# Kernel tuning notes

Hardware: AMD Instinct MI355X
Metric: run time of the kernel (lower is better)

Reference implementation:

```python
import jax, jax.numpy as jnp
import numpy as np

B, T, S, A, H = 64, 128, 100, 16, 120
TAU = 5.0


def setup_inputs() -> dict:
    key = jax.random.key(0)
    ks = jax.random.split(key, 12)
    kH = 1.0 / np.sqrt(H)
    u = lambda k, shape, b: jax.random.uniform(k, shape, jnp.float32, -b, b)
    return {
        "x": jax.random.normal(ks[0], (B, T, S, A), jnp.float32),
        # PyTorch LSTM params (gate order i, f, g, o), uniform(-1/sqrt(H), 1/sqrt(H))
        "W_ih": u(ks[1], (4 * H, A), kH),
        "W_hh": u(ks[2], (4 * H, H), kH),
        "b_ih": u(ks[3], (4 * H,), kH),
        "b_hh": u(ks[4], (4 * H,), kH),
        # score head: Linear(H, 1)
        "w_lin": u(ks[5], (1, H), kH),
        "b_lin": u(ks[6], (1,), kH),
        # MLP: Linear(S*S, 256), Linear(256, S)
        "W2": u(ks[7], (256, S * S), 1.0 / np.sqrt(S * S)),
        "b2": u(ks[8], (256,), 1.0 / np.sqrt(S * S)),
        "W3": u(ks[9], (S, 256), 1.0 / np.sqrt(256)),
        "b3": u(ks[10], (S,), 1.0 / np.sqrt(256)),
    }


def reference(x, W_ih, W_hh, b_ih, b_hh, w_lin, b_lin, W2, b2, W3, b3):
    Bsz, Tlen, Ns, _ = x.shape
    Hd = W_hh.shape[1]
    # Batch all stocks together: original loops the LSTM per stock with zero init,
    # which is mathematically identical to one LSTM over batch B*S.
    xr = jnp.transpose(x, (1, 0, 2, 3)).reshape(Tlen, Bsz * Ns, -1)  # (T, B*S, A)
    bias = b_ih + b_hh

    def step(carry, xt):
        h, c = carry
        g = xt @ W_ih.T + h @ W_hh.T + bias          # (B*S, 4H)
        i, f, gg, o = jnp.split(g, 4, axis=-1)
        i = jax.nn.sigmoid(i)
        f = jax.nn.sigmoid(f)
        gg = jnp.tanh(gg)
        o = jax.nn.sigmoid(o)
        c = f * c + i * gg
        h = o * jnp.tanh(c)
        return (h, c), None

    h0 = jnp.zeros((Bsz * Ns, Hd), x.dtype)
    (h_last, _), _ = jax.lax.scan(step, (h0, h0), xr)
    lstm_out_last = h_last.reshape(Bsz, Ns, Hd)       # (B, S, H)

    # per-element score linear (batched instead of python double-loop)
    s = lstm_out_last @ w_lin.T + b_lin               # (B, S, 1)

    # NeuralSort relaxed permutation matrix, tau = 5
    A_s = jnp.abs(s - jnp.transpose(s, (0, 2, 1)))    # (B, S, S)
    rowsum = A_s.sum(axis=-1, keepdims=True)          # (B, S, 1) == A_s @ 1 1^T rows
    scaling = (Ns + 1 - 2 * jnp.arange(1, Ns + 1)).astype(x.dtype)  # (S,)
    C = s * scaling[None, None, :]                    # (B, S, S)
    P_max = jnp.transpose(C - rowsum, (0, 2, 1))
    p_hat = jax.nn.softmax(P_max / TAU, axis=-1)      # (B, S, S)

    foo = p_hat.reshape(Bsz, Ns * Ns)
    z = jax.nn.relu(foo @ W2.T + b2)
    z = z @ W3.T + b3
    return jax.nn.softmax(z, axis=-1)                 # (B, S)
```

## Files before the change

kernel.cpp:

```cpp
#include <hip/hip_runtime.h>
#include <hip/hip_bf16.h>
#include <cstddef>

#define NSTOCK 100
#define LOG2E 1.4426950408889634f

typedef _Float16 f16x8 __attribute__((ext_vector_type(8)));
typedef _Float16 f16x4 __attribute__((ext_vector_type(4)));
typedef float f32x16 __attribute__((ext_vector_type(16)));

static __device__ __forceinline__ float rcpf(float x){ return __builtin_amdgcn_rcpf(x); }
static __device__ __forceinline__ float exp2f_(float x){ return __builtin_amdgcn_exp2f(x); }

__global__ void prep_kernel(const float* __restrict__ W_ih,
                            const float* __restrict__ W_hh,
                            const float* __restrict__ b_ih,
                            const float* __restrict__ b_hh,
                            float* __restrict__ Wp) {
    int idx = blockIdx.x * 256 + threadIdx.x;
    if (idx < 480 * 144) {
        int k = idx % 144;
        int p = idx / 144;
        int n = p >> 5, row = p & 31, jjf = row >> 2, type = row & 3;
        int j = n * 8 + (jjf & 1) * 4 + (jjf >> 1);
        int g = type * 120 + j;
        float scale = (type == 2) ? 2.f * LOG2E : -LOG2E;
        float v = 0.f;
        if (k < 136)       v = ((k < 16) ? W_ih[g * 16 + k] : W_hh[g * 120 + (k - 16)]) * scale;
        else if (k == 136) v = (b_ih[g] + b_hh[g]) * scale;
        Wp[idx] = v;
    }
}

__global__ __launch_bounds__(1024) void lstm_kernel(
        const float* __restrict__ x,
        const float* __restrict__ Wp,
        const float* __restrict__ w_lin,
        const float* __restrict__ b_lin,
        float* __restrict__ s_out) {
    __shared__ __align__(16) _Float16 AHi[2][9][64][8];
    __shared__ __align__(16) _Float16 ALoX[2][64][8];
    __shared__ float sred[30][32];

    const int tid   = threadIdx.x;
    const int lane  = tid & 63;
    const int w     = tid >> 6;
    const int l31   = lane & 31;
    const int lhalf = lane >> 5;
    const int n0    = blockIdx.x * 32;

    f16x8 bh[9], bl0;
    if (w < 15) {
        const int p = w * 32 + l31;
#pragma unroll
        for (int kt = 0; kt < 9; ++kt) {
            const float* wp = Wp + p * 144 + kt * 16 + lhalf * 8;
            f16x8 hi, lo;
#pragma unroll
            for (int e = 0; e < 8; ++e) {
                float v = wp[e];
                _Float16 h_ = (_Float16)v;
                hi[e] = h_;
                lo[e] = (_Float16)(v - (float)h_);
            }
            bh[kt] = hi;
            if (kt == 0) bl0 = lo;
        }
    }

    {
        f16x8 z;
#pragma unroll
        for (int e = 0; e < 8; ++e) z[e] = (_Float16)0.f;
        int bf = tid >> 9, kt = 1 + ((tid >> 6) & 7), ln = tid & 63;
        *(f16x8*)&AHi[bf][kt][ln][0] = z;
    }
    __syncthreads();

    const int bx = lane >> 1;
    const int hx = lane & 1;
    const int nx  = n0 + bx;
    const int bbx = nx / NSTOCK, ssx = nx % NSTOCK;
    const float* xbase = x + (size_t)bbx * 204800 + ssx * 16 + hx * 8;
    if (w == 15) {
        float4 a0 = *(const float4*)xbase;
        float4 a1 = *(const float4*)(xbase + 4);
        float vv[8] = {a0.x, a0.y, a0.z, a0.w, a1.x, a1.y, a1.z, a1.w};
        f16x8 hi, lo;
#pragma unroll
        for (int e = 0; e < 8; ++e) {
            _Float16 h_ = (_Float16)vv[e];
            hi[e] = h_; lo[e] = (_Float16)(vv[e] - (float)h_);
        }
        *(f16x8*)&AHi[0][0][bx + 32 * hx][0] = hi;
        *(f16x8*)&ALoX[0][bx + 32 * hx][0] = lo;
    }
    if (tid < 64) {
        int buf = tid >> 5, b = tid & 31;
        AHi[buf][8][32 + b][0] = (_Float16)1.f;
    }
    __syncthreads();

    const int ktw = 1 + (w >> 1);
    const int lnw = l31 + 32 * (w & 1);
    const int e0  = 4 * lhalf;

    float creg[4] = {0.f, 0.f, 0.f, 0.f};
    float hlast[4] = {0.f, 0.f, 0.f, 0.f};

    for (int t = 0; t < 128; ++t) {
        const int rb = t & 1;
        const int wb = rb ^ 1;
        if (w == 15) {
            int tt = (t < 127) ? t + 1 : 127;
            const float* xp = xbase + (size_t)tt * 1600;
            float4 a0 = *(const float4*)xp;
            float4 a1 = *(const float4*)(xp + 4);
            float vv[8] = {a0.x, a0.y, a0.z, a0.w, a1.x, a1.y, a1.z, a1.w};
            f16x8 hi, lo;
#pragma unroll
            for (int e = 0; e < 8; ++e) {
                _Float16 h_ = (_Float16)vv[e];
                hi[e] = h_; lo[e] = (_Float16)(vv[e] - (float)h_);
            }
            *(f16x8*)&AHi[wb][0][bx + 32 * hx][0] = hi;
            *(f16x8*)&ALoX[wb][bx + 32 * hx][0] = lo;
        } else {
            f32x16 acc;
#pragma unroll
            for (int r = 0; r < 16; ++r) acc[r] = 0.f;
            {
                f16x8 ah = *(const f16x8*)&AHi[rb][0][lane][0];
                f16x8 al = *(const f16x8*)&ALoX[rb][lane][0];
                acc = __builtin_amdgcn_mfma_f32_32x32x16_f16(bh[0], ah, acc, 0, 0, 0);
                acc = __builtin_amdgcn_mfma_f32_32x32x16_f16(bh[0], al, acc, 0, 0, 0);
                acc = __builtin_amdgcn_mfma_f32_32x32x16_f16(bl0, ah, acc, 0, 0, 0);
            }
#pragma unroll
            for (int kt = 1; kt < 9; ++kt) {
                f16x8 ah = *(const f16x8*)&AHi[rb][kt][lane][0];
                acc = __builtin_amdgcn_mfma_f32_32x32x16_f16(bh[kt], ah, acc, 0, 0, 0);
            }
            f16x4 hi4;
#pragma unroll
            for (int p = 0; p < 4; ++p) {
                float iv = rcpf(1.f + exp2f_(acc[4 * p + 0]));
                float fv = rcpf(1.f + exp2f_(acc[4 * p + 1]));
                float gv = 1.f - 2.f * rcpf(1.f + exp2f_(acc[4 * p + 2]));
                float ov = rcpf(1.f + exp2f_(acc[4 * p + 3]));
                float c = fv * creg[p] + iv * gv;
                creg[p] = c;
                float h = ov * (1.f - 2.f * rcpf(1.f + exp2f_(c * 2.8853900817779268f)));
                hlast[p] = h;
                hi4[p] = (_Float16)h;
            }
            *(f16x4*)&AHi[wb][ktw][lnw][e0] = hi4;
        }
        __syncthreads();
    }

    if (w < 15) {
        const int jb = w * 8 + 4 * lhalf;
        float sp = 0.f;
#pragma unroll
        for (int p = 0; p < 4; ++p) sp += w_lin[jb + p] * hlast[p];
        sred[w * 2 + lhalf][l31] = sp;
    }
    __syncthreads();
    if (tid < 32) {
        float s = b_lin[0];
#pragma unroll
        for (int r = 0; r < 30; ++r) s += sred[r][tid];
        s_out[n0 + tid] = s;
    }
}

__global__ __launch_bounds__(128) void phat_kernel(const float* __restrict__ s,
                                                   float* __restrict__ fooT) {
    __shared__ float a[NSTOCK], c[NSTOCK];
    const int b = blockIdx.x >> 1, half = blockIdx.x & 1, tid = threadIdx.x;
    const float* sb = s + b * NSTOCK;
    if (tid < NSTOCK) {
        float sj = sb[tid];
        float rs = 0.f;
        for (int i2 = 0; i2 < NSTOCK; ++i2) rs += fabsf(sj - sb[i2]);
        a[tid] = sj * 0.2f;
        c[tid] = rs * 0.2f;
    }
    __syncthreads();
    if (tid < 50) {
        const int i = half * 50 + tid;
        const float sci = (float)(99 - 2 * i);
        float m = -1e30f;
        for (int j = 0; j < NSTOCK; ++j) m = fmaxf(m, sci * a[j] - c[j]);
        float sum = 0.f;
        for (int j = 0; j < NSTOCK; ++j) sum += __expf(sci * a[j] - c[j] - m);
        const float inv = 1.f / sum;
        for (int j = 0; j < NSTOCK; ++j)
            fooT[(size_t)(i * NSTOCK + j) * 64 + b] = __expf(sci * a[j] - c[j] - m) * inv;
    }
}

__global__ __launch_bounds__(512) void mlp1_kernel(const float* __restrict__ fooT,
                                                   const float* __restrict__ W2,
                                                   float* __restrict__ z2Tp) {
    __shared__ float part[8][4][64];
    const int tid = threadIdx.x;
    const int wv = tid >> 6, lane = tid & 63;
    const int ug = blockIdx.x >> 1, half = blockIdx.x & 1;
    const int u0 = ug * 4;
    const int m0 = half * 5000 + wv * 625;
    float a0 = 0.f, a1 = 0.f, a2 = 0.f, a3 = 0.f;
    for (int mi = 0; mi < 625; ++mi) {
        int m = m0 + mi;
        float v = fooT[(size_t)m * 64 + lane];
        a0 += v * W2[(size_t)(u0 + 0) * 10000 + m];
        a1 += v * W2[(size_t)(u0 + 1) * 10000 + m];
        a2 += v * W2[(size_t)(u0 + 2) * 10000 + m];
        a3 += v * W2[(size_t)(u0 + 3) * 10000 + m];
    }
    part[wv][0][lane] = a0; part[wv][1][lane] = a1;
    part[wv][2][lane] = a2; part[wv][3][lane] = a3;
    __syncthreads();
    if (tid < 256) {
        int q = tid >> 6, b = tid & 63;
        float s = 0.f;
#pragma unroll
        for (int w2 = 0; w2 < 8; ++w2) s += part[w2][q][b];
        z2Tp[((size_t)half * 256 + (u0 + q)) * 64 + b] = s;
    }
}

__global__ __launch_bounds__(128) void mlp2_kernel(const float* __restrict__ z2Tp,
                                                   const float* __restrict__ b2,
                                                   const float* __restrict__ W3,
                                                   const float* __restrict__ b3,
                                                   float* __restrict__ out) {
    __shared__ float zs[256];
    __shared__ float logits[NSTOCK];
    const int b = blockIdx.x, tid = threadIdx.x;
    for (int u = tid; u < 256; u += 128) {
        float v = b2[u] + z2Tp[(size_t)u * 64 + b] + z2Tp[(size_t)(256 + u) * 64 + b];
        zs[u] = fmaxf(v, 0.f);
    }
    __syncthreads();
    if (tid < NSTOCK) {
        float acc = b3[tid];
        const float* wr = W3 + tid * 256;
        for (int u = 0; u < 256; ++u) acc += zs[u] * wr[u];
        logits[tid] = acc;
    }
    __syncthreads();
    if (tid < NSTOCK) {
        float m = -1e30f;
        for (int j = 0; j < NSTOCK; ++j) m = fmaxf(m, logits[j]);
        float sum = 0.f;
        for (int j = 0; j < NSTOCK; ++j) sum += __expf(logits[j] - m);
        out[b * NSTOCK + tid] = __expf(logits[tid] - m) / sum;
    }
}

extern "C" void kernel_launch(void* const* d_in, const int* in_sizes, int n_in,
                              void* d_out, int out_size, void* d_ws, size_t ws_size,
                              hipStream_t stream) {
    const float* x     = (const float*)d_in[0];
    const float* W_ih  = (const float*)d_in[1];
    const float* W_hh  = (const float*)d_in[2];
    const float* b_ih  = (const float*)d_in[3];
    const float* b_hh  = (const float*)d_in[4];
    const float* w_lin = (const float*)d_in[5];
    const float* b_lin = (const float*)d_in[6];
    const float* W2    = (const float*)d_in[7];
    const float* b2    = (const float*)d_in[8];
    const float* W3    = (const float*)d_in[9];
    const float* b3    = (const float*)d_in[10];

    float* ws    = (float*)d_ws;
    float* Wp    = ws;
    float* sbuf  = ws + 69600;
    float* fooT  = ws + 76000;
    float* z2Tp  = ws + 716000;
    float* out   = (float*)d_out;

    prep_kernel<<<271, 256, 0, stream>>>(W_ih, W_hh, b_ih, b_hh, Wp);
    lstm_kernel<<<200, 1024, 0, stream>>>(x, Wp, w_lin, b_lin, sbuf);
    phat_kernel<<<128, 128, 0, stream>>>(sbuf, fooT);
    mlp1_kernel<<<128, 512, 0, stream>>>(fooT, W2, z2Tp);
    mlp2_kernel<<<64, 128, 0, stream>>>(z2Tp, b2, W3, b3, out);
}
```

Measured before the change: 254.6 us.

## Interleave two sequence groups per LSTM block and restructure NeuralSort and MLP kernels

The LSTM kernel now processes 64 sequences per block as two independent 32-row groups. Their MFMA chains and gate math interleave, which gives ILP to hide MFMA latency within each serial timestep, and the grid halves to 100 blocks. The p_hat stage is split into a rowsum kernel and a per-row softmax kernel with coalesced 64-wide batch access, and it writes fooT in fp16 to halve traffic into mlp1. mlp1 computes 8 output units per block instead of 4, halving its grid and W2/fooT re-reads. The risks are fewer blocks on a large GPU (100 vs 200 CUs busy), higher register pressure, and fp16 rounding of the p_hat values.

```diff
diff --git a/kernel.cpp b/kernel.cpp
--- a/kernel.cpp
+++ b/kernel.cpp
@@ -38,16 +38,16 @@
         const float* __restrict__ w_lin,
         const float* __restrict__ b_lin,
         float* __restrict__ s_out) {
-    __shared__ __align__(16) _Float16 AHi[2][9][64][8];
-    __shared__ __align__(16) _Float16 ALoX[2][64][8];
-    __shared__ float sred[30][32];
+    __shared__ __align__(16) _Float16 AHi[2][2][9][64][8];
+    __shared__ __align__(16) _Float16 ALoX[2][2][64][8];
+    __shared__ float sred[30][64];
 
     const int tid   = threadIdx.x;
     const int lane  = tid & 63;
     const int w     = tid >> 6;
     const int l31   = lane & 31;
     const int lhalf = lane >> 5;
-    const int n0    = blockIdx.x * 32;
+    const int n0    = blockIdx.x * 64;
 
     f16x8 bh[9], bl0;
     if (w < 15) {
@@ -72,32 +72,38 @@
         f16x8 z;
 #pragma unroll
         for (int e = 0; e < 8; ++e) z[e] = (_Float16)0.f;
-        int bf = tid >> 9, kt = 1 + ((tid >> 6) & 7), ln = tid & 63;
-        *(f16x8*)&AHi[bf][kt][ln][0] = z;
+        for (int ii = tid; ii < 2048; ii += 1024) {
+            int g = ii >> 10, bf = (ii >> 9) & 1, kt = 1 + ((ii >> 6) & 7), ln = ii & 63;
+            *(f16x8*)&AHi[g][bf][kt][ln][0] = z;
+        }
     }
     __syncthreads();
 
     const int bx = lane >> 1;
     const int hx = lane & 1;
-    const int nx  = n0 + bx;
-    const int bbx = nx / NSTOCK, ssx = nx % NSTOCK;
-    const float* xbase = x + (size_t)bbx * 204800 + ssx * 16 + hx * 8;
+    const int rA = n0 + bx, rB = n0 + 32 + bx;
+    const float* xbaseA = x + (size_t)(rA / NSTOCK) * 204800 + (rA % NSTOCK) * 16 + hx * 8;
+    const float* xbaseB = x + (size_t)(rB / NSTOCK) * 204800 + (rB % NSTOCK) * 16 + hx * 8;
     if (w == 15) {
-        float4 a0 = *(const float4*)xbase;
-        float4 a1 = *(const float4*)(xbase + 4);
-        float vv[8] = {a0.x, a0.y, a0.z, a0.w, a1.x, a1.y, a1.z, a1.w};
-        f16x8 hi, lo;
-#pragma unroll
-        for (int e = 0; e < 8; ++e) {
-            _Float16 h_ = (_Float16)vv[e];
-            hi[e] = h_; lo[e] = (_Float16)(vv[e] - (float)h_);
-        }
-        *(f16x8*)&AHi[0][0][bx + 32 * hx][0] = hi;
-        *(f16x8*)&ALoX[0][bx + 32 * hx][0] = lo;
-    }
-    if (tid < 64) {
-        int buf = tid >> 5, b = tid & 31;
-        AHi[buf][8][32 + b][0] = (_Float16)1.f;
+#pragma unroll
+        for (int g = 0; g < 2; ++g) {
+            const float* xb = g ? xbaseB : xbaseA;
+            float4 a0 = *(const float4*)xb;
+            float4 a1 = *(const float4*)(xb + 4);
+            float vv[8] = {a0.x, a0.y, a0.z, a0.w, a1.x, a1.y, a1.z, a1.w};
+            f16x8 hi, lo;
+#pragma unroll
+            for (int e = 0; e < 8; ++e) {
+                _Float16 h_ = (_Float16)vv[e];
+                hi[e] = h_; lo[e] = (_Float16)(vv[e] - (float)h_);
+            }
+            *(f16x8*)&AHi[g][0][0][bx + 32 * hx][0] = hi;
+            *(f16x8*)&ALoX[g][0][bx + 32 * hx][0] = lo;
+        }
+    }
+    if (tid < 128) {
+        int g = tid >> 6, buf = (tid >> 5) & 1, b = tid & 31;
+        AHi[g][buf][8][32 + b][0] = (_Float16)1.f;
     }
     __syncthreads();
 
@@ -105,69 +111,111 @@
     const int lnw = l31 + 32 * (w & 1);
     const int e0  = 4 * lhalf;
 
-    float creg[4] = {0.f, 0.f, 0.f, 0.f};
-    float hlast[4] = {0.f, 0.f, 0.f, 0.f};
+    float cregA[4] = {0.f, 0.f, 0.f, 0.f};
+    float cregB[4] = {0.f, 0.f, 0.f, 0.f};
+    float hlastA[4] = {0.f, 0.f, 0.f, 0.f};
+    float hlastB[4] = {0.f, 0.f, 0.f, 0.f};
 
     for (int t = 0; t < 128; ++t) {
         const int rb = t & 1;
         const int wb = rb ^ 1;
         if (w == 15) {
             int tt = (t < 127) ? t + 1 : 127;
-            const float* xp = xbase + (size_t)tt * 1600;
-            float4 a0 = *(const float4*)xp;
-            float4 a1 = *(const float4*)(xp + 4);
-            float vv[8] = {a0.x, a0.y, a0.z, a0.w, a1.x, a1.y, a1.z, a1.w};
-            f16x8 hi, lo;
-#pragma unroll
-            for (int e = 0; e < 8; ++e) {
-                _Float16 h_ = (_Float16)vv[e];
-                hi[e] = h_; lo[e] = (_Float16)(vv[e] - (float)h_);
-            }
-            *(f16x8*)&AHi[wb][0][bx + 32 * hx][0] = hi;
-            *(f16x8*)&ALoX[wb][bx + 32 * hx][0] = lo;
+#pragma unroll
+            for (int g = 0; g < 2; ++g) {
+                const float* xp = (g ? xbaseB : xbaseA) + (size_t)tt * 1600;
+                float4 a0 = *(const float4*)xp;
+                float4 a1 = *(const float4*)(xp + 4);
+                float vv[8] = {a0.x, a0.y, a0.z, a0.w, a1.x, a1.y, a1.z, a1.w};
+                f16x8 hi, lo;
+#pragma unroll
+                for (int e = 0; e < 8; ++e) {
+                    _Float16 h_ = (_Float16)vv[e];
+                    hi[e] = h_; lo[e] = (_Float16)(vv[e] - (float)h_);
+                }
+                *(f16x8*)&AHi[g][wb][0][bx + 32 * hx][0] = hi;
+                *(f16x8*)&ALoX[g][wb][bx + 32 * hx][0] = lo;
+            }
         } else {
-            f32x16 acc;
-#pragma unroll
-            for (int r = 0; r < 16; ++r) acc[r] = 0.f;
+            f32x16 accA;
+#pragma unroll
+            for (int r = 0; r < 16; ++r) accA[r] = 0.f;
             {
-                f16x8 ah = *(const f16x8*)&AHi[rb][0][lane][0];
-                f16x8 al = *(const f16x8*)&ALoX[rb][lane][0];
-                acc = __builtin_amdgcn_mfma_f32_32x32x16_f16(bh[0], ah, acc, 0, 0, 0);
-                acc = __builtin_amdgcn_mfma_f32_32x32x16_f16(bh[0], al, acc, 0, 0, 0);
-                acc = __builtin_amdgcn_mfma_f32_32x32x16_f16(bl0, ah, acc, 0, 0, 0);
+                f16x8 ah = *(const f16x8*)&AHi[0][rb][0][lane][0];
+                f16x8 al = *(const f16x8*)&ALoX[0][rb][lane][0];
+                accA = __builtin_amdgcn_mfma_f32_32x32x16_f16(bh[0], ah, accA, 0, 0, 0);
+                accA = __builtin_amdgcn_mfma_f32_32x32x16_f16(bh[0], al, accA, 0, 0, 0);
+                accA = __builtin_amdgcn_mfma_f32_32x32x16_f16(bl0, ah, accA, 0, 0, 0);
             }
 #pragma unroll
             for (int kt = 1; kt < 9; ++kt) {
-                f16x8 ah = *(const f16x8*)&AHi[rb][kt][lane][0];
-                acc = __builtin_amdgcn_mfma_f32_32x32x16_f16(bh[kt], ah, acc, 0, 0, 0);
-            }
-            f16x4 hi4;
-#pragma unroll
-            for (int p = 0; p < 4; ++p) {
-                float iv = rcpf(1.f + exp2f_(acc[4 * p + 0]));
-                float fv = rcpf(1.f + exp2f_(acc[4 * p + 1]));
-                float gv = 1.f - 2.f * rcpf(1.f + exp2f_(acc[4 * p + 2]));
-                float ov = rcpf(1.f + exp2f_(acc[4 * p + 3]));
-                float c = fv * creg[p] + iv * gv;
-                creg[p] = c;
-                float h = ov * (1.f - 2.f * rcpf(1.f + exp2f_(c * 2.8853900817779268f)));
-                hlast[p] = h;
-                hi4[p] = (_Float16)h;
-            }
-            *(f16x4*)&AHi[wb][ktw][lnw][e0] = hi4;
+                f16x8 ah = *(const f16x8*)&AHi[0][rb][kt][lane][0];
+                accA = __builtin_amdgcn_mfma_f32_32x32x16_f16(bh[kt], ah, accA, 0, 0, 0);
+            }
+            f32x16 accB;
+#pragma unroll
+            for (int r = 0; r < 16; ++r) accB[r] = 0.f;
+            {
+                f16x8 ah = *(const f16x8*)&AHi[1][rb][0][lane][0];
+                f16x8 al = *(const f16x8*)&ALoX[1][rb][lane][0];
+                accB = __builtin_amdgcn_mfma_f32_32x32x16_f16(bh[0], ah, accB, 0, 0, 0);
+                accB = __builtin_amdgcn_mfma_f32_32x32x16_f16(bh[0], al, accB, 0, 0, 0);
+                accB = __builtin_amdgcn_mfma_f32_32x32x16_f16(bl0, ah, accB, 0, 0, 0);
+            }
+#pragma unroll
+            for (int kt = 1; kt < 9; ++kt) {
+                f16x8 ah = *(const f16x8*)&AHi[1][rb][kt][lane][0];
+                accB = __builtin_amdgcn_mfma_f32_32x32x16_f16(bh[kt], ah, accB, 0, 0, 0);
+            }
+            {
+                f16x4 hi4;
+#pragma unroll
+                for (int p = 0; p < 4; ++p) {
+                    float iv = rcpf(1.f + exp2f_(accA[4 * p + 0]));
+                    float fv = rcpf(1.f + exp2f_(accA[4 * p + 1]));
+                    float gv = 1.f - 2.f * rcpf(1.f + exp2f_(accA[4 * p + 2]));
+                    float ov = rcpf(1.f + exp2f_(accA[4 * p + 3]));
+                    float c = fv * cregA[p] + iv * gv;
+                    cregA[p] = c;
+                    float h = ov * (1.f - 2.f * rcpf(1.f + exp2f_(c * 2.8853900817779268f)));
+                    hlastA[p] = h;
+                    hi4[p] = (_Float16)h;
+                }
+                *(f16x4*)&AHi[0][wb][ktw][lnw][e0] = hi4;
+            }
+            {
+                f16x4 hi4;
+#pragma unroll
+                for (int p = 0; p < 4; ++p) {
+                    float iv = rcpf(1.f + exp2f_(accB[4 * p + 0]));
+                    float fv = rcpf(1.f + exp2f_(accB[4 * p + 1]));
+                    float gv = 1.f - 2.f * rcpf(1.f + exp2f_(accB[4 * p + 2]));
+                    float ov = rcpf(1.f + exp2f_(accB[4 * p + 3]));
+                    float c = fv * cregB[p] + iv * gv;
+                    cregB[p] = c;
+                    float h = ov * (1.f - 2.f * rcpf(1.f + exp2f_(c * 2.8853900817779268f)));
+                    hlastB[p] = h;
+                    hi4[p] = (_Float16)h;
+                }
+                *(f16x4*)&AHi[1][wb][ktw][lnw][e0] = hi4;
+            }
         }
         __syncthreads();
     }
 
     if (w < 15) {
         const int jb = w * 8 + 4 * lhalf;
-        float sp = 0.f;
-#pragma unroll
-        for (int p = 0; p < 4; ++p) sp += w_lin[jb + p] * hlast[p];
-        sred[w * 2 + lhalf][l31] = sp;
-    }
-    __syncthreads();
-    if (tid < 32) {
+        float spA = 0.f, spB = 0.f;
+#pragma unroll
+        for (int p = 0; p < 4; ++p) {
+            spA += w_lin[jb + p] * hlastA[p];
+            spB += w_lin[jb + p] * hlastB[p];
+        }
+        sred[w * 2 + lhalf][l31] = spA;
+        sred[w * 2 + lhalf][32 + l31] = spB;
+    }
+    __syncthreads();
+    if (tid < 64) {
         float s = b_lin[0];
 #pragma unroll
         for (int r = 0; r < 30; ++r) s += sred[r][tid];
@@ -175,54 +223,63 @@
     }
 }
 
-__global__ __launch_bounds__(128) void phat_kernel(const float* __restrict__ s,
-                                                   float* __restrict__ fooT) {
-    __shared__ float a[NSTOCK], c[NSTOCK];
-    const int b = blockIdx.x >> 1, half = blockIdx.x & 1, tid = threadIdx.x;
-    const float* sb = s + b * NSTOCK;
+__global__ __launch_bounds__(128) void rowsum_kernel(const float* __restrict__ s,
+                                                     float* __restrict__ aT,
+                                                     float* __restrict__ cT) {
+    __shared__ float sb[NSTOCK];
+    const int b = blockIdx.x, tid = threadIdx.x;
+    if (tid < NSTOCK) sb[tid] = s[b * NSTOCK + tid];
+    __syncthreads();
     if (tid < NSTOCK) {
         float sj = sb[tid];
         float rs = 0.f;
         for (int i2 = 0; i2 < NSTOCK; ++i2) rs += fabsf(sj - sb[i2]);
-        a[tid] = sj * 0.2f;
-        c[tid] = rs * 0.2f;
-    }
-    __syncthreads();
-    if (tid < 50) {
-        const int i = half * 50 + tid;
-        const float sci = (float)(99 - 2 * i);
-        float m = -1e30f;
-        for (int j = 0; j < NSTOCK; ++j) m = fmaxf(m, sci * a[j] - c[j]);
-        float sum = 0.f;
-        for (int j = 0; j < NSTOCK; ++j) sum += __expf(sci * a[j] - c[j] - m);
-        const float inv = 1.f / sum;
-        for (int j = 0; j < NSTOCK; ++j)
-            fooT[(size_t)(i * NSTOCK + j) * 64 + b] = __expf(sci * a[j] - c[j] - m) * inv;
-    }
-}
-
-__global__ __launch_bounds__(512) void mlp1_kernel(const float* __restrict__ fooT,
+        aT[tid * 64 + b] = sj * 0.2f;
+        cT[tid * 64 + b] = rs * 0.2f;
+    }
+}
+
+__global__ __launch_bounds__(64) void phat_kernel(const float* __restrict__ aT,
+                                                  const float* __restrict__ cT,
+                                                  _Float16* __restrict__ fooT16) {
+    const int i = blockIdx.x, b = threadIdx.x;
+    const float sci = (float)(99 - 2 * i);
+    float m = -1e30f;
+    for (int j = 0; j < NSTOCK; ++j)
+        m = fmaxf(m, sci * aT[j * 64 + b] - cT[j * 64 + b]);
+    float sum = 0.f;
+    for (int j = 0; j < NSTOCK; ++j)
+        sum += __expf(sci * aT[j * 64 + b] - cT[j * 64 + b] - m);
+    const float inv = 1.f / sum;
+    for (int j = 0; j < NSTOCK; ++j) {
+        float v = __expf(sci * aT[j * 64 + b] - cT[j * 64 + b] - m) * inv;
+        fooT16[(size_t)(i * NSTOCK + j) * 64 + b] = (_Float16)v;
+    }
+}
+
+__global__ __launch_bounds__(512) void mlp1_kernel(const _Float16* __restrict__ fooT16,
                                                    const float* __restrict__ W2,
                                                    float* __restrict__ z2Tp) {
-    __shared__ float part[8][4][64];
+    __shared__ float part[8][8][64];
     const int tid = threadIdx.x;
     const int wv = tid >> 6, lane = tid & 63;
     const int ug = blockIdx.x >> 1, half = blockIdx.x & 1;
-    const int u0 = ug * 4;
+    const int u0 = ug * 8;
     const int m0 = half * 5000 + wv * 625;
-    float a0 = 0.f, a1 = 0.f, a2 = 0.f, a3 = 0.f;
+    float a[8];
+#pragma unroll
+    for (int q = 0; q < 8; ++q) a[q] = 0.f;
     for (int mi = 0; mi < 625; ++mi) {
         int m = m0 + mi;
-        float v = fooT[(size_t)m * 64 + lane];
-        a0 += v * W2[(size_t)(u0 + 0) * 10000 + m];
-        a1 += v * W2[(size_t)(u0 + 1) * 10000 + m];
-        a2 += v * W2[(size_t)(u0 + 2) * 10000 + m];
-        a3 += v * W2[(size_t)(u0 + 3) * 10000 + m];
-    }
-    part[wv][0][lane] = a0; part[wv][1][lane] = a1;
-    part[wv][2][lane] = a2; part[wv][3][lane] = a3;
-    __syncthreads();
-    if (tid < 256) {
+        float v = (float)fooT16[(size_t)m * 64 + lane];
+#pragma unroll
+        for (int q = 0; q < 8; ++q)
+            a[q] += v * W2[(size_t)(u0 + q) * 10000 + m];
+    }
+#pragma unroll
+    for (int q = 0; q < 8; ++q) part[wv][q][lane] = a[q];
+    __syncthreads();
+    {
         int q = tid >> 6, b = tid & 63;
         float s = 0.f;
 #pragma unroll
@@ -278,13 +335,16 @@
     float* ws    = (float*)d_ws;
     float* Wp    = ws;
     float* sbuf  = ws + 69600;
-    float* fooT  = ws + 76000;
-    float* z2Tp  = ws + 716000;
+    float* aT    = ws + 76000;
+    float* cT    = ws + 82400;
+    _Float16* fooT16 = (_Float16*)(ws + 88800);
+    float* z2Tp  = ws + 408800;
     float* out   = (float*)d_out;
 
     prep_kernel<<<271, 256, 0, stream>>>(W_ih, W_hh, b_ih, b_hh, Wp);
-    lstm_kernel<<<200, 1024, 0, stream>>>(x, Wp, w_lin, b_lin, sbuf);
-    phat_kernel<<<128, 128, 0, stream>>>(sbuf, fooT);
-    mlp1_kernel<<<128, 512, 0, stream>>>(fooT, W2, z2Tp);
+    lstm_kernel<<<100, 1024, 0, stream>>>(x, Wp, w_lin, b_lin, sbuf);
+    rowsum_kernel<<<64, 128, 0, stream>>>(sbuf, aT, cT);
+    phat_kernel<<<100, 64, 0, stream>>>(aT, cT, fooT16);
+    mlp1_kernel<<<64, 512, 0, stream>>>(fooT16, W2, z2Tp);
     mlp2_kernel<<<64, 128, 0, stream>>>(z2Tp, b2, W3, b3, out);
 }
```

Result: slower. 506.8 us (+99.0%).
